# Optimization experiments

Measured on AMD Instinct MI355X. Metric: run time of the kernel, lower is better.

## Reference

```python
import jax, jax.numpy as jnp
import numpy as np

B, S = 8, 128
D_SENS, D_ACT, D_STR, D_ENC, DIM = 512, 32, 128, 128, 128
D_JOINT = D_STR + D_ENC  # 256


def _l2norm(x):
    return x / jnp.clip(jnp.linalg.norm(x, axis=-1, keepdims=True), 1e-12)


def _mlp(x, layers):
    # layers: list of (W, b); ReLU between layers, none on output
    n = len(layers)
    for i, (W, b) in enumerate(layers):
        x = x @ W + b
        if i < n - 1:
            x = jax.nn.relu(x)
    return x


def _meta_mlp(x, p):
    x = jax.nn.relu(x @ p['W1'] + p['b1'])
    x = jax.nn.relu(x @ p['W2'] + p['b2'])
    return x @ p['W3'] + p['b3']


def setup_inputs() -> dict:
    key = jax.random.key(0)
    it = iter(jax.random.split(key, 40))
    w = lambda shape, s=0.02: jax.random.normal(next(it), shape, jnp.float32) * s
    H = D_ACT * 4  # to_transitions hidden dim (default mlp_hidden_dim)
    return dict(
        sensory=jax.random.normal(next(it), (B, S, D_SENS), jnp.float32),
        actions=jax.random.normal(next(it), (B, S, D_ACT), jnp.float32),
        init_hidden=w((1, D_STR), 0.01),
        tW1=w((D_ACT, H)), tb1=w((H,)),
        tW2=w((H, H)), tb2=w((H,)),
        tW3=w((H, D_STR * D_STR)), tb3=w((D_STR * D_STR,)),
        enc_w=w((D_SENS, D_ENC)), enc_b=w((D_ENC,)),
        dec_w=w((D_ENC, D_SENS)), dec_b=w((D_SENS,)),
        q_w=w((D_JOINT, DIM)), k_w=w((D_JOINT, DIM)), v_w=w((D_JOINT, DIM)),
        mW1=w((DIM, 2 * DIM)), mb1=w((2 * DIM,)),
        mW2=w((2 * DIM, 2 * DIM)), mb2=w((2 * DIM,)),
        mW3=w((2 * DIM, DIM)), mb3=w((DIM,)),
        oW1=w((DIM, 2 * DIM)), ob1=w((2 * DIM,)),
        oW2=w((2 * DIM, 2 * DIM)), ob2=w((2 * DIM,)),
        oW3=w((2 * DIM, D_JOINT)), ob3=w((D_JOINT,)),
        sW1=w((2 * D_STR + 1, 2 * D_STR)), sb1=w((2 * D_STR,)),
        sW2=w((2 * D_STR, 2 * D_STR)), sb2=w((2 * D_STR,)),
        sW3=w((2 * D_STR, D_STR)), sb3=w((D_STR,)),
        integration_ratio=jnp.asarray(0.1, jnp.float32),
    )


def reference(sensory, actions, init_hidden, tW1, tb1, tW2, tb2, tW3, tb3,
              enc_w, enc_b, dec_w, dec_b, q_w, k_w, v_w,
              mW1, mb1, mW2, mb2, mW3, mb3,
              oW1, ob1, oW2, ob2, oW3, ob3,
              sW1, sb1, sW2, sb2, sW3, sb3, integration_ratio):
    mse = lambda a, b: jnp.mean((a - b) ** 2)

    # --- PathIntegration: actions -> transitions -> scripted RNN scan ---
    trans = _mlp(actions, [(tW1, tb1), (tW2, tb2), (tW3, tb3)])  # (B,S,ds*ds)
    trans = trans.reshape(B, S, D_STR, D_STR)
    h0 = jnp.broadcast_to(_l2norm(init_hidden), (B, D_STR))

    def step(h, T):  # h (B,ds), T (B,ds,ds)
        h = _l2norm(jax.nn.relu(jnp.einsum('bi,bij->bj', h, T)))
        return h, h

    _, hs = jax.lax.scan(step, h0, jnp.swapaxes(trans, 0, 1))
    structural = jnp.swapaxes(hs, 0, 1)  # (B,S,ds)

    # --- sensory encoder (Linear) ---
    encoded = sensory @ enc_w + enc_b  # (B,S,D_ENC)

    meta_params = {'W1': mW1, 'b1': mb1, 'W2': mW2, 'b2': mb2, 'W3': mW3, 'b3': mb3}

    def retrieve(s, e):
        joint = jnp.concatenate((s, e), axis=-1)
        q = joint @ q_w
        r = _meta_mlp(q, meta_params)
        out = _mlp(r, [(oW1, ob1), (oW2, ob2), (oW3, ob3)])
        return out[..., :D_STR], out[..., D_STR:]

    # generative branch
    dec_gen_s, dec_enc = retrieve(structural, jnp.zeros_like(encoded))
    generative_pred_loss = mse(sensory, dec_enc @ dec_w + dec_b)

    # relational branch (source calls retrieve(zeros, encoded) twice)
    dec_s1, _ = retrieve(jnp.zeros_like(structural), encoded)
    dec_s2, _ = retrieve(jnp.zeros_like(structural), encoded)
    relational_loss = mse(dec_s1, structural) + mse(dec_s2, structural)

    # consistency / inference correction
    corr_s, corr_e = retrieve(dec_gen_s, encoded)
    sse = jnp.sum((corr_e - encoded) ** 2, axis=-1, keepdims=True)  # (B,S,1)
    pred_var = _mlp(jnp.concatenate((corr_s, dec_gen_s, sse), axis=-1),
                    [(sW1, sb1), (sW2, sb2), (sW3, sb3)])
    inf_s = dec_gen_s + (corr_s - dec_gen_s) * integration_ratio * pred_var
    consistency_loss = mse(dec_gen_s, inf_s)

    final_s, inf_e = retrieve(inf_s, jnp.zeros_like(encoded))
    inference_pred_loss = mse(sensory, inf_e @ dec_w + dec_b)

    # per-sample fast-weight memory gradients (nested vmap(grad))
    store = jnp.concatenate((final_s, encoded), axis=-1)
    keys = store @ k_w
    values = store @ v_w

    def meta_loss(p, k, v):
        return jnp.mean((_meta_mlp(k, p) - v) ** 2)

    per_grad = jax.vmap(jax.vmap(jax.grad(meta_loss), in_axes=(None, 0, 0)),
                        in_axes=(None, 0, 0))
    g = per_grad(meta_params, keys, values)  # each leaf (B,S,*param_shape)

    total = (generative_pred_loss + relational_loss
             + consistency_loss + inference_pred_loss)  # all loss weights 1.0
    return (total, g['W1'], g['b1'], g['W2'], g['b2'], g['W3'], g['b3'])
```

## Files before the change

### kernel.cpp

```cpp
#include <hip/hip_runtime.h>
#include <hip/hip_bf16.h>

constexpr size_t OFF_W1 = 1;
constexpr size_t OFF_B1 = OFF_W1 + (size_t)1024*32768;
constexpr size_t OFF_W2 = OFF_B1 + (size_t)1024*256;
constexpr size_t OFF_B2 = OFF_W2 + (size_t)1024*65536;
constexpr size_t OFF_W3 = OFF_B2 + (size_t)1024*256;
constexpr size_t OFF_B3 = OFF_W3 + (size_t)1024*32768;

__device__ __forceinline__ void layer_n256_r8(
    const float* __restrict__ W, const float* __restrict__ bias, int K,
    const float* __restrict__ x, int xs, float* __restrict__ y, int relu, int t)
{
    const int c4 = (t & 63) * 4;
    const int r0 = (t >> 6) * 2;
    float4 a0 = bias ? *(const float4*)&bias[c4] : make_float4(0.f,0.f,0.f,0.f);
    float4 a1 = a0;
    const float* x0 = x + r0 * xs;
    const float* x1 = x0 + xs;
    for (int k = 0; k < K; ++k) {
        float4 w = *(const float4*)&W[(size_t)k*256 + c4];
        float xa = x0[k], xb = x1[k];
        a0.x = fmaf(w.x, xa, a0.x); a0.y = fmaf(w.y, xa, a0.y);
        a0.z = fmaf(w.z, xa, a0.z); a0.w = fmaf(w.w, xa, a0.w);
        a1.x = fmaf(w.x, xb, a1.x); a1.y = fmaf(w.y, xb, a1.y);
        a1.z = fmaf(w.z, xb, a1.z); a1.w = fmaf(w.w, xb, a1.w);
    }
    if (relu) {
        a0.x=fmaxf(a0.x,0.f); a0.y=fmaxf(a0.y,0.f); a0.z=fmaxf(a0.z,0.f); a0.w=fmaxf(a0.w,0.f);
        a1.x=fmaxf(a1.x,0.f); a1.y=fmaxf(a1.y,0.f); a1.z=fmaxf(a1.z,0.f); a1.w=fmaxf(a1.w,0.f);
    }
    *(float4*)&y[r0*256 + c4] = a0;
    *(float4*)&y[(r0+1)*256 + c4] = a1;
}

__device__ __forceinline__ void layer_n256_r4(
    const float* __restrict__ W, const float* __restrict__ bias, int K,
    const float* __restrict__ x, int xs, float* __restrict__ y, int relu,
    const float* __restrict__ mask, int t)
{
    const int c4 = (t & 63) * 4;
    const int r = t >> 6;
    float4 a = bias ? *(const float4*)&bias[c4] : make_float4(0.f,0.f,0.f,0.f);
    const float* xr = x + r * xs;
    for (int k = 0; k < K; ++k) {
        float4 w = *(const float4*)&W[(size_t)k*256 + c4];
        float xa = xr[k];
        a.x = fmaf(w.x, xa, a.x); a.y = fmaf(w.y, xa, a.y);
        a.z = fmaf(w.z, xa, a.z); a.w = fmaf(w.w, xa, a.w);
    }
    if (relu) {
        a.x=fmaxf(a.x,0.f); a.y=fmaxf(a.y,0.f); a.z=fmaxf(a.z,0.f); a.w=fmaxf(a.w,0.f);
    }
    if (mask) {
        float4 m = *(const float4*)&mask[r*256 + c4];
        a.x = (m.x > 0.f) ? a.x : 0.f; a.y = (m.y > 0.f) ? a.y : 0.f;
        a.z = (m.z > 0.f) ? a.z : 0.f; a.w = (m.w > 0.f) ? a.w : 0.f;
    }
    *(float4*)&y[r*256 + c4] = a;
}

__device__ __forceinline__ void layer_n128(
    const float* __restrict__ W, const float* __restrict__ bias, int K,
    const float* __restrict__ x, int xs, float* __restrict__ y, int ys, int relu,
    int rows, int t)
{
    const int c4 = (t & 31) * 4;
    int r = t >> 5; if (rows == 4) r &= 3;
    float4 a = bias ? *(const float4*)&bias[c4] : make_float4(0.f,0.f,0.f,0.f);
    const float* xr = x + r * xs;
    for (int k = 0; k < K; ++k) {
        float4 w = *(const float4*)&W[(size_t)k*128 + c4];
        float xa = xr[k];
        a.x = fmaf(w.x, xa, a.x); a.y = fmaf(w.y, xa, a.y);
        a.z = fmaf(w.z, xa, a.z); a.w = fmaf(w.w, xa, a.w);
    }
    if (relu) {
        a.x=fmaxf(a.x,0.f); a.y=fmaxf(a.y,0.f); a.z=fmaxf(a.z,0.f); a.w=fmaxf(a.w,0.f);
    }
    *(float4*)&y[r*ys + c4] = a;
}

__device__ __forceinline__ void layer_n128_dual(
    const float* __restrict__ W,
    const float* __restrict__ xA, const float* __restrict__ xB,
    float* __restrict__ y, int rows, int t)
{
    const int c4 = (t & 31) * 4;
    int r = t >> 5; if (rows == 4) r &= 3;
    float4 a = make_float4(0.f,0.f,0.f,0.f);
    const float* xa_ = xA + r * 128;
    const float* xb_ = xB + r * 128;
    for (int k = 0; k < 128; ++k) {
        float4 w = *(const float4*)&W[(size_t)k*128 + c4];
        float v = xa_[k];
        a.x = fmaf(w.x, v, a.x); a.y = fmaf(w.y, v, a.y);
        a.z = fmaf(w.z, v, a.z); a.w = fmaf(w.w, v, a.w);
    }
    for (int k = 0; k < 128; ++k) {
        float4 w = *(const float4*)&W[(size_t)(128+k)*128 + c4];
        float v = xb_[k];
        a.x = fmaf(w.x, v, a.x); a.y = fmaf(w.y, v, a.y);
        a.z = fmaf(w.z, v, a.z); a.w = fmaf(w.w, v, a.w);
    }
    *(float4*)&y[r*128 + c4] = a;
}

__device__ __forceinline__ void block_mse_commit(float s, float scale,
                                                 float* __restrict__ accum,
                                                 float* __restrict__ red, int t)
{
    #pragma unroll
    for (int off = 32; off > 0; off >>= 1) s += __shfl_down(s, off, 64);
    if ((t & 63) == 0) red[t >> 6] = s;
    __syncthreads();
    if (t == 0) atomicAdd(accum, (red[0]+red[1]+red[2]+red[3]) * scale);
}

__device__ __forceinline__ void dec_mse(
    const float* __restrict__ ret,
    const float* __restrict__ sensory, int row0,
    const float* __restrict__ dec_w, const float* __restrict__ dec_b,
    float* __restrict__ accum, float* __restrict__ red, int t)
{
    const int c4 = (t & 127) * 4;
    const int rb = (t >> 7) * 2;
    float4 a0 = *(const float4*)&dec_b[c4];
    float4 a1 = a0;
    const float* x0 = ret + rb*256 + 128;
    const float* x1 = x0 + 256;
    for (int k = 0; k < 128; ++k) {
        float4 w = *(const float4*)&dec_w[(size_t)k*512 + c4];
        float xa = x0[k], xb = x1[k];
        a0.x = fmaf(w.x, xa, a0.x); a0.y = fmaf(w.y, xa, a0.y);
        a0.z = fmaf(w.z, xa, a0.z); a0.w = fmaf(w.w, xa, a0.w);
        a1.x = fmaf(w.x, xb, a1.x); a1.y = fmaf(w.y, xb, a1.y);
        a1.z = fmaf(w.z, xb, a1.z); a1.w = fmaf(w.w, xb, a1.w);
    }
    float4 s0 = *(const float4*)&sensory[(size_t)(row0+rb)*512 + c4];
    float4 s1 = *(const float4*)&sensory[(size_t)(row0+rb+1)*512 + c4];
    float dx0 = a0.x-s0.x, dy0 = a0.y-s0.y, dz0 = a0.z-s0.z, dw0 = a0.w-s0.w;
    float dx1 = a1.x-s1.x, dy1 = a1.y-s1.y, dz1 = a1.z-s1.z, dw1 = a1.w-s1.w;
    float s = dx0*dx0 + dy0*dy0 + dz0*dz0 + dw0*dw0
            + dx1*dx1 + dy1*dy1 + dz1*dz1 + dw1*dw1;
    block_mse_commit(s, 1.f/524288.f, accum, red, t);
}

__global__ __launch_bounds__(256) void prep_kernel(
    const float* __restrict__ tW3,
    const float* __restrict__ mW2, const float* __restrict__ mW3,
    const float* __restrict__ actions,
    const float* __restrict__ tW1, const float* __restrict__ tb1,
    const float* __restrict__ tW2, const float* __restrict__ tb2,
    const float* __restrict__ sensory,
    const float* __restrict__ enc_w, const float* __restrict__ enc_b,
    float* __restrict__ tW3T, float* __restrict__ T2, float* __restrict__ T3,
    float* __restrict__ acc, float* __restrict__ a2, float* __restrict__ encoded)
{
    __shared__ float smem[64*129];
    const int t = threadIdx.x;
    const int bid = blockIdx.x;
    if (bid < 256) {
        const int k = bid >> 1, i0 = (bid & 1) * 64;
        const size_t base = (size_t)k << 14;
        for (int l = t; l < 8192; l += 256) {
            int ii = l >> 7, jj = l & 127;
            smem[ii*129 + jj] = tW3[base + (size_t)(i0+ii)*128 + jj];
        }
        __syncthreads();
        for (int l = t; l < 8192; l += 256) {
            int jj = l >> 6, ii = l & 63;
            tW3T[base + (size_t)jj*128 + i0 + ii] = smem[ii*129 + jj];
        }
    } else if (bid < 512) {
        const int c = bid - 256;
        T2[(size_t)c*256 + t] = mW2[(size_t)t*256 + c];
    } else if (bid < 640) {
        const int c = bid - 512;
        T3[(size_t)c*256 + t] = mW3[(size_t)t*128 + c];
    } else if (bid == 640) {
        if (t < 16) acc[t] = 0.f;
    } else if (bid < 769) {
        float* bufAct = smem;
        float* ping   = smem + 256;
        float* pong   = smem + 1280;
        const int row0 = (bid - 641) * 8;
        if (t < 64) {
            int r = t >> 3, c4 = (t & 7) * 4;
            *(float4*)&bufAct[r*32 + c4] =
                *(const float4*)&actions[(size_t)(row0 + r)*32 + c4];
        }
        __syncthreads();
        layer_n128(tW1, tb1, 32, bufAct, 32, ping, 128, 1, 8, t);
        __syncthreads();
        layer_n128(tW2, tb2, 128, ping, 128, pong, 128, 1, 8, t);
        __syncthreads();
        {
            int r = t >> 5, c4 = (t & 31) * 4;
            *(float4*)&a2[(size_t)(row0 + r)*128 + c4] = *(const float4*)&pong[r*128 + c4];
        }
    } else {
        const int q = bid - 769;
        const int m0 = (q & 15) * 64, n0 = (q >> 4) * 64;
        float (*As)[65] = (float(*)[65])smem;
        float (*Ws)[65] = (float(*)[65])(smem + 16*65);
        const int tx = t & 15, ty = t >> 4;
        float a4[4][4] = {};
        for (int k0 = 0; k0 < 512; k0 += 16) {
            for (int l = t; l < 1024; l += 256) {
                int mm = l >> 4, kk = l & 15;
                As[kk][mm] = sensory[(size_t)(m0+mm)*512 + k0 + kk];
            }
            for (int l = t; l < 1024; l += 256) {
                int kk = l >> 6, nn = l & 63;
                Ws[kk][nn] = enc_w[(size_t)(k0+kk)*128 + n0 + nn];
            }
            __syncthreads();
            #pragma unroll
            for (int kk = 0; kk < 16; ++kk) {
                float a[4], b[4];
                #pragma unroll
                for (int i=0;i<4;i++) a[i] = As[kk][ty*4+i];
                #pragma unroll
                for (int j=0;j<4;j++) b[j] = Ws[kk][tx*4+j];
                #pragma unroll
                for (int i=0;i<4;i++)
                    #pragma unroll
                    for (int j=0;j<4;j++)
// ... 60 lines not shown
}

__global__ __launch_bounds__(512) void scanrel_kernel(
    const float* __restrict__ transT,
    const float* __restrict__ init_hidden,
    float* __restrict__ structural,
    const float* __restrict__ encoded,
    const float* __restrict__ qw,
    const float* __restrict__ mW1, const float* __restrict__ mb1,
    const float* __restrict__ mW2, const float* __restrict__ mb2,
    const float* __restrict__ mW3, const float* __restrict__ mb3,
    const float* __restrict__ oW1, const float* __restrict__ ob1,
    const float* __restrict__ oW2, const float* __restrict__ ob2,
    const float* __restrict__ oW3, const float* __restrict__ ob3,
    float* __restrict__ out2)
{
    __shared__ float smem[5120];
    const int tid = threadIdx.x;
    if (blockIdx.x < 8) {
        float* h  = smem;
        float* ws = smem + 128;
        const int b = blockIdx.x;
        const int j = tid >> 2, p = tid & 3;
        const int i0 = p * 32;

        if (tid < 32) {
            float4 v = *(const float4*)&init_hidden[tid*4];
            float ss = v.x*v.x + v.y*v.y + v.z*v.z + v.w*v.w;
            ss += __shfl_xor(ss, 16); ss += __shfl_xor(ss, 8); ss += __shfl_xor(ss, 4);
            ss += __shfl_xor(ss, 2);  ss += __shfl_xor(ss, 1);
            float inv = 1.f / fmaxf(sqrtf(ss), 1e-12f);
            v.x *= inv; v.y *= inv; v.z *= inv; v.w *= inv;
            *(float4*)&h[tid*4] = v;
        }
        __syncthreads();

        const size_t bbase = ((size_t)b) << 21;
        const int lane_off = j*128 + i0;
        float4 cur[8], nxt[8];
        {
            const float* T0 = transT + bbase + lane_off;
            #pragma unroll
            for (int r = 0; r < 8; ++r) cur[r] = *(const float4*)&T0[r*4];
        }
        for (int t = 0; t < 128; ++t) {
            const int tn = (t < 127) ? t + 1 : 127;
            const float* Tn = transT + bbase + ((size_t)tn << 14) + lane_off;
            #pragma unroll
            for (int r = 0; r < 8; ++r) nxt[r] = *(const float4*)&Tn[r*4];

            float4 a = make_float4(0.f, 0.f, 0.f, 0.f);
            #pragma unroll
            for (int r = 0; r < 8; ++r) {
                float4 hv = *(const float4*)&h[i0 + r*4];
                a.x = fmaf(hv.x, cur[r].x, a.x);
                a.y = fmaf(hv.y, cur[r].y, a.y);
                a.z = fmaf(hv.z, cur[r].z, a.z);
                a.w = fmaf(hv.w, cur[r].w, a.w);
            }
            float s = (a.x + a.y) + (a.z + a.w);
            s += __shfl_xor(s, 1);
            s += __shfl_xor(s, 2);
            float v = fmaxf(s, 0.f);
            float q = v * v;
            q += __shfl_xor(q, 4);  q += __shfl_xor(q, 8);
            q += __shfl_xor(q, 16); q += __shfl_xor(q, 32);
            if ((tid & 63) == 0) ws[tid >> 6] = q;
            __syncthreads();
            float ss = ((ws[0]+ws[1]) + (ws[2]+ws[3])) + ((ws[4]+ws[5]) + (ws[6]+ws[7]));
            float inv = 1.f / fmaxf(sqrtf(ss), 1e-12f);
            float hv = v * inv;
            __syncthreads();
            if (p == 0) h[j] = hv;
            else if (p == 1) structural[(((size_t)(b*128 + t)) << 7) + j] = hv;
            __syncthreads();
            #pragma unroll
            for (int r = 0; r < 8; ++r) cur[r] = nxt[r];
        }
    } else {
        float* bufB = smem;
        float* ping = smem + 1024;
        float* pong = smem + 3072;
        const int row0 = (blockIdx.x - 8) * 8;
        const bool act = (tid < 256);
        const int t = tid;
        if (act) {
            int r = t >> 5, k4 = (t & 31) * 4;
            *(float4*)&bufB[r*128 + k4] =
                *(const float4*)&encoded[(size_t)(row0 + r)*128 + k4];
        }
        __syncthreads();
        if (act) layer_n128(qw + (size_t)128*128, nullptr, 128, bufB, 128, ping, 128, 0, 8, t);
        __syncthreads();
        if (act) layer_n256_r8(mW1, mb1, 128, ping, 128, pong, 1, t);
        __syncthreads();
        if (act) layer_n256_r8(mW2, mb2, 256, pong, 256, ping, 1, t);
        __syncthreads();
        if (act) layer_n128(mW3, mb3, 256, ping, 256, pong, 128, 0, 8, t);
        __syncthreads();
        if (act) layer_n256_r8(oW1, ob1, 128, pong, 128, ping, 1, t);
        __syncthreads();
        if (act) layer_n256_r8(oW2, ob2, 256, ping, 256, pong, 1, t);
        __syncthreads();
        if (act) layer_n256_r8(oW3, ob3, 256, pong, 256, ping, 0, t);
        __syncthreads();
        if (act) {
            for (int e = t; e < 512; e += 256) {
                int r = e >> 6, c = (e & 63) * 4;
                *(float4*)&out2[(size_t)(row0+r)*256 + c] = *(const float4*)&ping[r*256 + c];
            }
        }
    }
}

__global__ __launch_bounds__(256) void mega_kernel(
    const float* __restrict__ structural, const float* __restrict__ encoded,
    const float* __restrict__ out2, const float* __restrict__ sensory,
    const float* __restrict__ ratio_p,
    const float* __restrict__ qw,
    const float* __restrict__ mW1, const float* __restrict__ mb1,
    const float* __restrict__ mW2, const float* __restrict__ mb2,
    const float* __restrict__ mW3, const float* __restrict__ mb3,
    const float* __restrict__ oW1, const float* __restrict__ ob1,
    const float* __restrict__ oW2, const float* __restrict__ ob2,
    const float* __restrict__ oW3, const float* __restrict__ ob3,
    const float* __restrict__ sW1, const float* __restrict__ sb1,
    const float* __restrict__ sW2, const float* __restrict__ sb2,
    const float* __restrict__ sW3, const float* __restrict__ sb3,
    const float* __restrict__ k_w, const float* __restrict__ v_w,
    const float* __restrict__ T2, const float* __restrict__ T3,
    const float* __restrict__ dec_w, const float* __restrict__ dec_b,
    float* __restrict__ acc, float* __restrict__ out)
{
    __shared__ float smem[9736];
    float* enc_s    = smem;
    float* struct_s = smem + 512;
    float* ping     = smem + 1024;
    float* pong     = smem + 2048;
    float* ret1     = smem + 3072;
    float* xa128    = smem + 4096;
    float* out3_s   = smem + 4608;
    float* pvar_s   = smem + 5632;
    float* infs_s   = smem + 6144;
    float* ks       = smem + 6656;
    float* vs       = smem + 7168;
    float* h1       = smem + 7680;
    float* h2       = smem + 8704;
    float* sse      = smem + 9728;
    float* red      = smem + 9732;
    const int t = threadIdx.x;
    const int row0 = blockIdx.x * 4;

    {
        int r = (t >> 5) & 3, k4 = (t & 31) * 4;
        *(float4*)&struct_s[r*128 + k4] = *(const float4*)&structural[(size_t)(row0+r)*128 + k4];
        *(float4*)&enc_s[r*128 + k4]    = *(const float4*)&encoded[(size_t)(row0+r)*128 + k4];
    }
    __syncthreads();
    layer_n128(qw, nullptr, 128, struct_s, 128, ping, 128, 0, 4, t); __syncthreads();
    layer_n256_r4(mW1, mb1, 128, ping, 128, pong, 1, nullptr, t); __syncthreads();
    layer_n256_r4(mW2, mb2, 256, pong, 256, ping, 1, nullptr, t); __syncthreads();
    layer_n128(mW3, mb3, 256, ping, 256, pong, 128, 0, 4, t); __syncthreads();
    layer_n256_r4(oW1, ob1, 128, pong, 128, ping, 1, nullptr, t); __syncthreads();
    layer_n256_r4(oW2, ob2, 256, ping, 256, pong, 1, nullptr, t); __syncthreads();
    layer_n256_r4(oW3, ob3, 256, pong, 256, ret1, 0, nullptr, t); __syncthreads();
    {
        float relsum = 0.f;
        for (int e = t; e < 512; e += 256) {
            int r = e >> 7, c = e & 127;
            xa128[e] = ret1[r*256 + c];
            float d = out2[(size_t)(row0+r)*256 + c] - struct_s[r*128 + c];
            relsum = fmaf(d, d, relsum);
        }
        block_mse_commit(relsum, 2.f/131072.f, acc + 1, red, t);
    }
    __syncthreads();
    dec_mse(ret1, sensory, row0, dec_w, dec_b, acc + 0, red, t);
    __syncthreads();
    layer_n128_dual(qw, xa128, enc_s, ping, 4, t); __syncthreads();
    layer_n256_r4(mW1, mb1, 128, ping, 128, pong, 1, nullptr, t); __syncthreads();
    layer_n256_r4(mW2, mb2, 256, pong, 256, ping, 1, nullptr, t); __syncthreads();
    layer_n128(mW3, mb3, 256, ping, 256, pong, 128, 0, 4, t); __syncthreads();
    layer_n256_r4(oW1, ob1, 128, pong, 128, ping, 1, nullptr, t); __syncthreads();
    layer_n256_r4(oW2, ob2, 256, ping, 256, pong, 1, nullptr, t); __syncthreads();
    layer_n256_r4(oW3, ob3, 256, pong, 256, out3_s, 0, nullptr, t); __syncthreads();
    {
        int r = (t >> 5) & 3, k4 = (t & 31) * 4;
        float4 ce = *(const float4*)&out3_s[r*256 + 128 + k4];
        float4 en = *(const float4*)&enc_s[r*128 + k4];
        float dx = ce.x-en.x, dy = ce.y-en.y, dz = ce.z-en.z, dw = ce.w-en.w;
        float ss = dx*dx + dy*dy + dz*dz + dw*dw;
        ss += __shfl_xor(ss, 16); ss += __shfl_xor(ss, 8); ss += __shfl_xor(ss, 4);
        ss += __shfl_xor(ss, 2);  ss += __shfl_xor(ss, 1);
        if ((t & 31) == 0) sse[r] = ss;
    }
    __syncthreads();
    {
        const int c4 = (t & 63) * 4;
        const int r = t >> 6;
        float4 a = *(const float4*)&sb1[c4];
        for (int k = 0; k < 128; ++k) {
            float4 w = *(const float4*)&sW1[(size_t)k*256 + c4];
            float xa = out3_s[r*256 + k];
            a.x=fmaf(w.x,xa,a.x); a.y=fmaf(w.y,xa,a.y); a.z=fmaf(w.z,xa,a.z); a.w=fmaf(w.w,xa,a.w);
        }
        for (int k = 0; k < 128; ++k) {
            float4 w = *(const float4*)&sW1[(size_t)(128+k)*256 + c4];
            float xa = xa128[r*128 + k];
            a.x=fmaf(w.x,xa,a.x); a.y=fmaf(w.y,xa,a.y); a.z=fmaf(w.z,xa,a.z); a.w=fmaf(w.w,xa,a.w);
        }
        {
            float4 w = *(const float4*)&sW1[(size_t)256*256 + c4];
            float xa = sse[r];
            a.x=fmaf(w.x,xa,a.x); a.y=fmaf(w.y,xa,a.y); a.z=fmaf(w.z,xa,a.z); a.w=fmaf(w.w,xa,a.w);
        }
        a.x=fmaxf(a.x,0.f); a.y=fmaxf(a.y,0.f); a.z=fmaxf(a.z,0.f); a.w=fmaxf(a.w,0.f);
        *(float4*)&ping[r*256 + c4] = a;
    }
    __syncthreads();
    layer_n256_r4(sW2, sb2, 256, ping, 256, pong, 1, nullptr, t); __syncthreads();
    layer_n128(sW3, sb3, 256, pong, 256, pvar_s, 128, 0, 4, t); __syncthreads();
    {
        float ratio = ratio_p[0];
        float ssum = 0.f;
        for (int e = t; e < 512; e += 256) {
            int r = e >> 7, j = e & 127;
            float dgs = xa128[r*128 + j];
            float cs  = out3_s[r*256 + j];
            float pv  = pvar_s[r*128 + j];
            float delta = (cs - dgs) * ratio * pv;
            infs_s[r*128 + j] = dgs + delta;
            ssum = fmaf(delta, delta, ssum);
        }
        block_mse_commit(ssum, 1.f/131072.f, acc + 2, red, t);
    }
    __syncthreads();
    layer_n128(qw, nullptr, 128, infs_s, 128, ping, 128, 0, 4, t); __syncthreads();
    layer_n256_r4(mW1, mb1, 128, ping, 128, pong, 1, nullptr, t); __syncthreads();
    layer_n256_r4(mW2, mb2, 256, pong, 256, ping, 1, nullptr, t); __syncthreads();
    layer_n128(mW3, mb3, 256, ping, 256, pong, 128, 0, 4, t); __syncthreads();
    layer_n256_r4(oW1, ob1, 128, pong, 128, ping, 1, nullptr, t); __syncthreads();
    layer_n256_r4(oW2, ob2, 256, ping, 256, pong, 1, nullptr, t); __syncthreads();
    layer_n256_r4(oW3, ob3, 256, pong, 256, ret1, 0, nullptr, t); __syncthreads();
    dec_mse(ret1, sensory, row0, dec_w, dec_b, acc + 3, red, t);
    __syncthreads();
    for (int e = t; e < 512; e += 256) {
        int r = e >> 7, c = e & 127;
        xa128[e] = ret1[r*256 + c];
    }
    __syncthreads();
    float* dob = pvar_s;
    float* dh2 = out3_s;
    float* dh1 = ping;
    layer_n128_dual(k_w, xa128, enc_s, ks, 4, t);
    layer_n128_dual(v_w, xa128, enc_s, vs, 4, t);
    __syncthreads();
    layer_n256_r4(mW1, mb1, 128, ks, 128, h1, 1, nullptr, t);
    __syncthreads();
    layer_n256_r4(mW2, mb2, 256, h1, 256, h2, 1, nullptr, t);
    __syncthreads();
    layer_n128(mW3, mb3, 256, h2, 256, dob, 128, 0, 4, t);
    __syncthreads();
    for (int e = t; e < 512; e += 256)
        dob[e] = (dob[e] - vs[e]) * 0.015625f;
    __syncthreads();
    layer_n256_r4(T3, nullptr, 128, dob, 128, dh2, 0, h2, t);
    __syncthreads();
    layer_n256_r4(T2, nullptr, 256, dh2, 256, dh1, 0, h1, t);
    __syncthreads();
    #pragma unroll
    for (int r = 0; r < 4; ++r) {
        const size_t row = row0 + r;
        {
            const int c4 = (t & 63) * 4;
            const int i0 = (t >> 6) * 32;
            const float4 dv = *(const float4*)&dh1[r*256 + c4];
            float* p = out + OFF_W1 + row*32768;
            for (int i = i0; i < i0 + 32; ++i) {
                float kv = ks[r*128 + i];
                float4 o; o.x = kv*dv.x; o.y = kv*dv.y; o.z = kv*dv.z; o.w = kv*dv.w;
                *(float4*)&p[(size_t)i*256 + c4] = o;
            }
            out[OFF_B1 + row*256 + t] = dh1[r*256 + t];
        }
        {
            const int c4 = (t & 63) * 4;
            const int i0 = (t >> 6) * 64;
            const float4 dv = *(const float4*)&dh2[r*256 + c4];
            float* p = out + OFF_W2 + row*65536;
            for (int i = i0; i < i0 + 64; ++i) {
                float hv = h1[r*256 + i];
                float4 o; o.x = hv*dv.x; o.y = hv*dv.y; o.z = hv*dv.z; o.w = hv*dv.w;
                *(float4*)&p[(size_t)i*256 + c4] = o;
            }
            out[OFF_B2 + row*256 + t] = dh2[r*256 + t];
        }
        {
            const int c4 = (t & 31) * 4;
            const int i0 = (t >> 5) * 32;
            const float4 dv = *(const float4*)&dob[r*128 + c4];
            float* p = out + OFF_W3 + row*32768;
            for (int i = i0; i < i0 + 32; ++i) {
                float hv = h2[r*256 + i];
                float4 o; o.x = hv*dv.x; o.y = hv*dv.y; o.z = hv*dv.z; o.w = hv*dv.w;
                *(float4*)&p[(size_t)i*128 + c4] = o;
            }
            if (t < 128) out[OFF_B3 + row*128 + t] = dob[r*128 + t];
        }
    }
}

__global__ void total_kernel(const float* acc, float* out) {
    if (threadIdx.x == 0)
        out[0] = acc[0] + acc[1] + acc[2] + acc[3];
}

extern "C" void kernel_launch(void* const* d_in, const int* in_sizes, int n_in,
                              void* d_out, int out_size, void* d_ws, size_t ws_size,
                              hipStream_t stream)
{
    const float* sensory     = (const float*)d_in[0];
    const float* actions     = (const float*)d_in[1];
    const float* init_hidden = (const float*)d_in[2];
    const float* tW1 = (const float*)d_in[3];  const float* tb1 = (const float*)d_in[4];
    const float* tW2 = (const float*)d_in[5];  const float* tb2 = (const float*)d_in[6];
    const float* tW3 = (const float*)d_in[7];  const float* tb3 = (const float*)d_in[8];
    const float* enc_w = (const float*)d_in[9];  const float* enc_b = (const float*)d_in[10];
    const float* dec_w = (const float*)d_in[11]; const float* dec_b = (const float*)d_in[12];
    const float* q_w = (const float*)d_in[13];
    const float* k_w = (const float*)d_in[14];
    const float* v_w = (const float*)d_in[15];
    const float* mW1 = (const float*)d_in[16]; const float* mb1 = (const float*)d_in[17];
    const float* mW2 = (const float*)d_in[18]; const float* mb2 = (const float*)d_in[19];
    const float* mW3 = (const float*)d_in[20]; const float* mb3 = (const float*)d_in[21];
    const float* oW1 = (const float*)d_in[22]; const float* ob1 = (const float*)d_in[23];
    const float* oW2 = (const float*)d_in[24]; const float* ob2 = (const float*)d_in[25];
    const float* oW3 = (const float*)d_in[26]; const float* ob3 = (const float*)d_in[27];
    const float* sW1 = (const float*)d_in[28]; const float* sb1 = (const float*)d_in[29];
    const float* sW2 = (const float*)d_in[30]; const float* sb2 = (const float*)d_in[31];
    const float* sW3 = (const float*)d_in[32]; const float* sb3 = (const float*)d_in[33];
    const float* ratio = (const float*)d_in[34];
    float* out = (float*)d_out;

    float* Wsp = (float*)d_ws;
    float* acc   = Wsp;
    float* ALIAS = Wsp + 16;
    float* structural = ALIAS + 131072;
    float* out2 = ALIAS + 524288;
    float* tW3T = ALIAS;
    size_t off = 16 + 2097152;
    float* a2      = Wsp + off; off += 131072;
    float* encoded = Wsp + off; off += 131072;
    float* transT  = Wsp + off; off += 16777216;
    float* T2      = Wsp + off; off += 65536;
    float* T3      = Wsp + off; off += 32768;

    prep_kernel<<<801, 256, 0, stream>>>(tW3, mW2, mW3, actions, tW1, tb1, tW2, tb2,
                                         sensory, enc_w, enc_b, tW3T, T2, T3,
                                         acc, a2, encoded);

    gemm_k128_kernel<<<dim3(32, 64), 256, 0, stream>>>(a2, 128, tW3T, tb3, transT, 16384);

    scanrel_kernel<<<136, 512, 0, stream>>>(transT, init_hidden, structural, encoded,
        q_w, mW1, mb1, mW2, mb2, mW3, mb3, oW1, ob1, oW2, ob2, oW3, ob3, out2);

    mega_kernel<<<256, 256, 0, stream>>>(structural, encoded, out2, sensory, ratio,
        q_w, mW1, mb1, mW2, mb2, mW3, mb3, oW1, ob1, oW2, ob2, oW3, ob3,
        sW1, sb1, sW2, sb2, sW3, sb3, k_w, v_w, T2, T3, dec_w, dec_b, acc, out);

    total_kernel<<<1, 64, 0, stream>>>(acc, out);
}
```

Measured before the change: 1.321 ms.

## Double mega_kernel threads with split-K layers and widen scanrel MLP to 512 threads

Launches mega_kernel with 512 threads per block and splits each small MLP layer's K dimension across 2 or 4 thread groups, reducing partial sums through shared memory. In scanrel, the 8-row MLP layers now use all 512 threads, one row per thread, instead of 256 threads handling two rows each. The decoder MSE and the gradient outer-product writes are spread over the wider block. The aim is more latency hiding and parallelism on a grid of only 256 blocks, at the cost of extra shared memory, extra barriers and reduction work per layer.

```diff
diff --git a/kernel.cpp b/kernel.cpp
--- a/kernel.cpp
+++ b/kernel.cpp
@@ -8,36 +8,30 @@
 constexpr size_t OFF_W3 = OFF_B2 + (size_t)1024*256;
 constexpr size_t OFF_B3 = OFF_W3 + (size_t)1024*32768;
 
-__device__ __forceinline__ void layer_n256_r8(
+__device__ __forceinline__ void layer_n128(
+    const float* __restrict__ W, const float* __restrict__ bias, int K,
+    const float* __restrict__ x, int xs, float* __restrict__ y, int ys, int relu,
+    int rows, int t)
+{
+    const int c4 = (t & 31) * 4;
+    int r = t >> 5; if (rows == 4) r &= 3;
+    float4 a = bias ? *(const float4*)&bias[c4] : make_float4(0.f,0.f,0.f,0.f);
+    const float* xr = x + r * xs;
+    for (int k = 0; k < K; ++k) {
+        float4 w = *(const float4*)&W[(size_t)k*128 + c4];
+        float xa = xr[k];
+        a.x = fmaf(w.x, xa, a.x); a.y = fmaf(w.y, xa, a.y);
+        a.z = fmaf(w.z, xa, a.z); a.w = fmaf(w.w, xa, a.w);
+    }
+    if (relu) {
+        a.x=fmaxf(a.x,0.f); a.y=fmaxf(a.y,0.f); a.z=fmaxf(a.z,0.f); a.w=fmaxf(a.w,0.f);
+    }
+    *(float4*)&y[r*ys + c4] = a;
+}
+
+__device__ __forceinline__ void layer_n256_512(
     const float* __restrict__ W, const float* __restrict__ bias, int K,
     const float* __restrict__ x, int xs, float* __restrict__ y, int relu, int t)
-{
-    const int c4 = (t & 63) * 4;
-    const int r0 = (t >> 6) * 2;
-    float4 a0 = bias ? *(const float4*)&bias[c4] : make_float4(0.f,0.f,0.f,0.f);
-    float4 a1 = a0;
-    const float* x0 = x + r0 * xs;
-    const float* x1 = x0 + xs;
-    for (int k = 0; k < K; ++k) {
-        float4 w = *(const float4*)&W[(size_t)k*256 + c4];
-        float xa = x0[k], xb = x1[k];
-        a0.x = fmaf(w.x, xa, a0.x); a0.y = fmaf(w.y, xa, a0.y);
-        a0.z = fmaf(w.z, xa, a0.z); a0.w = fmaf(w.w, xa, a0.w);
-        a1.x = fmaf(w.x, xb, a1.x); a1.y = fmaf(w.y, xb, a1.y);
-        a1.z = fmaf(w.z, xb, a1.z); a1.w = fmaf(w.w, xb, a1.w);
-    }
-    if (relu) {
-        a0.x=fmaxf(a0.x,0.f); a0.y=fmaxf(a0.y,0.f); a0.z=fmaxf(a0.z,0.f); a0.w=fmaxf(a0.w,0.f);
-        a1.x=fmaxf(a1.x,0.f); a1.y=fmaxf(a1.y,0.f); a1.z=fmaxf(a1.z,0.f); a1.w=fmaxf(a1.w,0.f);
-    }
-    *(float4*)&y[r0*256 + c4] = a0;
-    *(float4*)&y[(r0+1)*256 + c4] = a1;
-}
-
-__device__ __forceinline__ void layer_n256_r4(
-    const float* __restrict__ W, const float* __restrict__ bias, int K,
-    const float* __restrict__ x, int xs, float* __restrict__ y, int relu,
-    const float* __restrict__ mask, int t)
 {
     const int c4 = (t & 63) * 4;
     const int r = t >> 6;
@@ -52,98 +46,159 @@
     if (relu) {
         a.x=fmaxf(a.x,0.f); a.y=fmaxf(a.y,0.f); a.z=fmaxf(a.z,0.f); a.w=fmaxf(a.w,0.f);
     }
-    if (mask) {
-        float4 m = *(const float4*)&mask[r*256 + c4];
-        a.x = (m.x > 0.f) ? a.x : 0.f; a.y = (m.y > 0.f) ? a.y : 0.f;
-        a.z = (m.z > 0.f) ? a.z : 0.f; a.w = (m.w > 0.f) ? a.w : 0.f;
-    }
     *(float4*)&y[r*256 + c4] = a;
 }
 
-__device__ __forceinline__ void layer_n128(
+__device__ __forceinline__ void layer_ks2_n256(
+    const float* __restrict__ W, const float* __restrict__ bias, int K,
+    const float* __restrict__ x, int xs, float* __restrict__ y, int relu,
+    const float* __restrict__ mask, float* __restrict__ part, int t)
+{
+    const int g = t >> 8;
+    const int tt = t & 255;
+    const int r = tt >> 6, c4 = (tt & 63) * 4;
+    const int kh = K >> 1;
+    const int kb = g * kh;
+    float4 a = make_float4(0.f,0.f,0.f,0.f);
+    const float* xr = x + r * xs;
+    for (int k = kb; k < kb + kh; ++k) {
+        float4 w = *(const float4*)&W[(size_t)k*256 + c4];
+        float xa = xr[k];
+        a.x = fmaf(w.x, xa, a.x); a.y = fmaf(w.y, xa, a.y);
+        a.z = fmaf(w.z, xa, a.z); a.w = fmaf(w.w, xa, a.w);
+    }
+    *(float4*)&part[g*1024 + tt*4] = a;
+    __syncthreads();
+    if (g == 0) {
+        float4 p0 = *(const float4*)&part[tt*4];
+        float4 p1 = *(const float4*)&part[1024 + tt*4];
+        float4 o;
+        o.x = p0.x + p1.x; o.y = p0.y + p1.y; o.z = p0.z + p1.z; o.w = p0.w + p1.w;
+        if (bias) {
+            float4 b = *(const float4*)&bias[c4];
+            o.x += b.x; o.y += b.y; o.z += b.z; o.w += b.w;
+        }
+        if (relu) {
+            o.x=fmaxf(o.x,0.f); o.y=fmaxf(o.y,0.f); o.z=fmaxf(o.z,0.f); o.w=fmaxf(o.w,0.f);
+        }
+        if (mask) {
+            float4 m = *(const float4*)&mask[r*256 + c4];
+            o.x = (m.x > 0.f) ? o.x : 0.f; o.y = (m.y > 0.f) ? o.y : 0.f;
+            o.z = (m.z > 0.f) ? o.z : 0.f; o.w = (m.w > 0.f) ? o.w : 0.f;
+        }
+        *(float4*)&y[r*256 + c4] = o;
+    }
+    __syncthreads();
+}
+
+__device__ __forceinline__ void layer_ks4_n128(
     const float* __restrict__ W, const float* __restrict__ bias, int K,
     const float* __restrict__ x, int xs, float* __restrict__ y, int ys, int relu,
-    int rows, int t)
-{
-    const int c4 = (t & 31) * 4;
-    int r = t >> 5; if (rows == 4) r &= 3;
-    float4 a = bias ? *(const float4*)&bias[c4] : make_float4(0.f,0.f,0.f,0.f);
+    float* __restrict__ part, int t)
+{
+    const int g = t >> 7;
+    const int tt = t & 127;
+    const int r = tt >> 5, c4 = (tt & 31) * 4;
+    const int kq = K >> 2;
+    const int kb = g * kq;
+    float4 a = make_float4(0.f,0.f,0.f,0.f);
     const float* xr = x + r * xs;
-    for (int k = 0; k < K; ++k) {
+    for (int k = kb; k < kb + kq; ++k) {
         float4 w = *(const float4*)&W[(size_t)k*128 + c4];
         float xa = xr[k];
         a.x = fmaf(w.x, xa, a.x); a.y = fmaf(w.y, xa, a.y);
         a.z = fmaf(w.z, xa, a.z); a.w = fmaf(w.w, xa, a.w);
     }
-    if (relu) {
-        a.x=fmaxf(a.x,0.f); a.y=fmaxf(a.y,0.f); a.z=fmaxf(a.z,0.f); a.w=fmaxf(a.w,0.f);
-    }
-    *(float4*)&y[r*ys + c4] = a;
-}
-
-__device__ __forceinline__ void layer_n128_dual(
+    *(float4*)&part[g*512 + tt*4] = a;
+    __syncthreads();
+    if (g == 0) {
+        float4 p0 = *(const float4*)&part[tt*4];
+        float4 p1 = *(const float4*)&part[512 + tt*4];
+        float4 p2 = *(const float4*)&part[1024 + tt*4];
+        float4 p3 = *(const float4*)&part[1536 + tt*4];
+        float4 o;
+        o.x = (p0.x+p1.x) + (p2.x+p3.x); o.y = (p0.y+p1.y) + (p2.y+p3.y);
+        o.z = (p0.z+p1.z) + (p2.z+p3.z); o.w = (p0.w+p1.w) + (p2.w+p3.w);
+        if (bias) {
+            float4 b = *(const float4*)&bias[c4];
+            o.x += b.x; o.y += b.y; o.z += b.z; o.w += b.w;
+        }
+        if (relu) {
+            o.x=fmaxf(o.x,0.f); o.y=fmaxf(o.y,0.f); o.z=fmaxf(o.z,0.f); o.w=fmaxf(o.w,0.f);
+        }
+        *(float4*)&y[r*ys + c4] = o;
+    }
+    __syncthreads();
+}
+
+__device__ __forceinline__ void layer_ks4_n128_dual(
     const float* __restrict__ W,
     const float* __restrict__ xA, const float* __restrict__ xB,
-    float* __restrict__ y, int rows, int t)
-{
-    const int c4 = (t & 31) * 4;
-    int r = t >> 5; if (rows == 4) r &= 3;
+    float* __restrict__ y, float* __restrict__ part, int t)
+{
+    const int g = t >> 7;
+    const int tt = t & 127;
+    const int r = tt >> 5, c4 = (tt & 31) * 4;
+    const float* src = (g < 2) ? xA : xB;
+    const int kb = (g & 1) * 64;
+    const int wb = g * 64;
     float4 a = make_float4(0.f,0.f,0.f,0.f);
-    const float* xa_ = xA + r * 128;
-    const float* xb_ = xB + r * 128;
-    for (int k = 0; k < 128; ++k) {
-        float4 w = *(const float4*)&W[(size_t)k*128 + c4];
-        float v = xa_[k];
-        a.x = fmaf(w.x, v, a.x); a.y = fmaf(w.y, v, a.y);
-        a.z = fmaf(w.z, v, a.z); a.w = fmaf(w.w, v, a.w);
-    }
-    for (int k = 0; k < 128; ++k) {
-        float4 w = *(const float4*)&W[(size_t)(128+k)*128 + c4];
-        float v = xb_[k];
-        a.x = fmaf(w.x, v, a.x); a.y = fmaf(w.y, v, a.y);
-        a.z = fmaf(w.z, v, a.z); a.w = fmaf(w.w, v, a.w);
-    }
-    *(float4*)&y[r*128 + c4] = a;
-}
-
-__device__ __forceinline__ void block_mse_commit(float s, float scale,
-                                                 float* __restrict__ accum,
-                                                 float* __restrict__ red, int t)
+    const float* xr = src + r * 128;
+    for (int k = 0; k < 64; ++k) {
+        float4 w = *(const float4*)&W[(size_t)(wb + k)*128 + c4];
+        float xa = xr[kb + k];
+        a.x = fmaf(w.x, xa, a.x); a.y = fmaf(w.y, xa, a.y);
+        a.z = fmaf(w.z, xa, a.z); a.w = fmaf(w.w, xa, a.w);
+    }
+    *(float4*)&part[g*512 + tt*4] = a;
+    __syncthreads();
+    if (g == 0) {
+        float4 p0 = *(const float4*)&part[tt*4];
+        float4 p1 = *(const float4*)&part[512 + tt*4];
+        float4 p2 = *(const float4*)&part[1024 + tt*4];
+        float4 p3 = *(const float4*)&part[1536 + tt*4];
+        float4 o;
+        o.x = (p0.x+p1.x) + (p2.x+p3.x); o.y = (p0.y+p1.y) + (p2.y+p3.y);
+        o.z = (p0.z+p1.z) + (p2.z+p3.z); o.w = (p0.w+p1.w) + (p2.w+p3.w);
+        *(float4*)&y[r*128 + c4] = o;
+    }
+    __syncthreads();
+}
+
+__device__ __forceinline__ void block_mse_commit512(float s, float scale,
+                                                    float* __restrict__ accum,
+                                                    float* __restrict__ red, int t)
 {
     #pragma unroll
     for (int off = 32; off > 0; off >>= 1) s += __shfl_down(s, off, 64);
     if ((t & 63) == 0) red[t >> 6] = s;
     __syncthreads();
-    if (t == 0) atomicAdd(accum, (red[0]+red[1]+red[2]+red[3]) * scale);
-}
-
-__device__ __forceinline__ void dec_mse(
+    if (t == 0) {
+        float tot = ((red[0]+red[1]) + (red[2]+red[3])) + ((red[4]+red[5]) + (red[6]+red[7]));
+        atomicAdd(accum, tot * scale);
+    }
+}
+
+__device__ __forceinline__ void dec_mse512(
     const float* __restrict__ ret,
     const float* __restrict__ sensory, int row0,
     const float* __restrict__ dec_w, const float* __restrict__ dec_b,
     float* __restrict__ accum, float* __restrict__ red, int t)
 {
     const int c4 = (t & 127) * 4;
-    const int rb = (t >> 7) * 2;
-    float4 a0 = *(const float4*)&dec_b[c4];
-    float4 a1 = a0;
+    const int rb = t >> 7;
+    float4 a = *(const float4*)&dec_b[c4];
     const float* x0 = ret + rb*256 + 128;
-    const float* x1 = x0 + 256;
     for (int k = 0; k < 128; ++k) {
         float4 w = *(const float4*)&dec_w[(size_t)k*512 + c4];
-        float xa = x0[k], xb = x1[k];
-        a0.x = fmaf(w.x, xa, a0.x); a0.y = fmaf(w.y, xa, a0.y);
-        a0.z = fmaf(w.z, xa, a0.z); a0.w = fmaf(w.w, xa, a0.w);
-        a1.x = fmaf(w.x, xb, a1.x); a1.y = fmaf(w.y, xb, a1.y);
-        a1.z = fmaf(w.z, xb, a1.z); a1.w = fmaf(w.w, xb, a1.w);
+        float xa = x0[k];
+        a.x = fmaf(w.x, xa, a.x); a.y = fmaf(w.y, xa, a.y);
+        a.z = fmaf(w.z, xa, a.z); a.w = fmaf(w.w, xa, a.w);
     }
     float4 s0 = *(const float4*)&sensory[(size_t)(row0+rb)*512 + c4];
-    float4 s1 = *(const float4*)&sensory[(size_t)(row0+rb+1)*512 + c4];
-    float dx0 = a0.x-s0.x, dy0 = a0.y-s0.y, dz0 = a0.z-s0.z, dw0 = a0.w-s0.w;
-    float dx1 = a1.x-s1.x, dy1 = a1.y-s1.y, dz1 = a1.z-s1.z, dw1 = a1.w-s1.w;
-    float s = dx0*dx0 + dy0*dy0 + dz0*dz0 + dw0*dw0
-            + dx1*dx1 + dy1*dy1 + dz1*dz1 + dw1*dw1;
-    block_mse_commit(s, 1.f/524288.f, accum, red, t);
+    float dx = a.x-s0.x, dy = a.y-s0.y, dz = a.z-s0.z, dw = a.w-s0.w;
+    float s = dx*dx + dy*dy + dz*dz + dw*dw;
+    block_mse_commit512(s, 1.f/524288.f, accum, red, t);
 }
 
 __global__ __launch_bounds__(256) void prep_kernel(
@@ -370,38 +425,35 @@
         float* ping = smem + 1024;
         float* pong = smem + 3072;
         const int row0 = (blockIdx.x - 8) * 8;
-        const bool act = (tid < 256);
         const int t = tid;
-        if (act) {
+        if (t < 256) {
             int r = t >> 5, k4 = (t & 31) * 4;
             *(float4*)&bufB[r*128 + k4] =
                 *(const float4*)&encoded[(size_t)(row0 + r)*128 + k4];
         }
         __syncthreads();
-        if (act) layer_n128(qw + (size_t)128*128, nullptr, 128, bufB, 128, ping, 128, 0, 8, t);
-        __syncthreads();
-        if (act) layer_n256_r8(mW1, mb1, 128, ping, 128, pong, 1, t);
-        __syncthreads();
-        if (act) layer_n256_r8(mW2, mb2, 256, pong, 256, ping, 1, t);
-        __syncthreads();
-        if (act) layer_n128(mW3, mb3, 256, ping, 256, pong, 128, 0, 8, t);
-        __syncthreads();
-        if (act) layer_n256_r8(oW1, ob1, 128, pong, 128, ping, 1, t);
-        __syncthreads();
-        if (act) layer_n256_r8(oW2, ob2, 256, ping, 256, pong, 1, t);
-        __syncthreads();
-        if (act) layer_n256_r8(oW3, ob3, 256, pong, 256, ping, 0, t);
-        __syncthreads();
-        if (act) {
-            for (int e = t; e < 512; e += 256) {
-                int r = e >> 6, c = (e & 63) * 4;
-                *(float4*)&out2[(size_t)(row0+r)*256 + c] = *(const float4*)&ping[r*256 + c];
-            }
-        }
-    }
-}
-
-__global__ __launch_bounds__(256) void mega_kernel(
+        if (t < 256) layer_n128(qw + (size_t)128*128, nullptr, 128, bufB, 128, ping, 128, 0, 8, t);
+        __syncthreads();
+        layer_n256_512(mW1, mb1, 128, ping, 128, pong, 1, t);
+        __syncthreads();
+        layer_n256_512(mW2, mb2, 256, pong, 256, ping, 1, t);
+        __syncthreads();
+        if (t < 256) layer_n128(mW3, mb3, 256, ping, 256, pong, 128, 0, 8, t);
+        __syncthreads();
+        layer_n256_512(oW1, ob1, 128, pong, 128, ping, 1, t);
+        __syncthreads();
+        layer_n256_512(oW2, ob2, 256, ping, 256, pong, 1, t);
+        __syncthreads();
+        layer_n256_512(oW3, ob3, 256, pong, 256, ping, 0, t);
+        __syncthreads();
+        {
+            int r = t >> 6, c = (t & 63) * 4;
+            *(float4*)&out2[(size_t)(row0+r)*256 + c] = *(const float4*)&ping[r*256 + c];
+        }
+    }
+}
+
+__global__ __launch_bounds__(512) void mega_kernel(
     const float* __restrict__ structural, const float* __restrict__ encoded,
     const float* __restrict__ out2, const float* __restrict__ sensory,
     const float* __restrict__ ratio_p,
@@ -420,7 +472,7 @@
     const float* __restrict__ dec_w, const float* __restrict__ dec_b,
     float* __restrict__ acc, float* __restrict__ out)
 {
-    __shared__ float smem[9736];
+    __shared__ float smem[11788];
     float* enc_s    = smem;
     float* struct_s = smem + 512;
     float* ping     = smem + 1024;
@@ -434,45 +486,43 @@
     float* vs       = smem + 7168;
     float* h1       = smem + 7680;
     float* h2       = smem + 8704;
-    float* sse      = smem + 9728;
-    float* red      = smem + 9732;
+    float* part     = smem + 9728;
+    float* sse      = smem + 11776;
+    float* red      = smem + 11780;
     const int t = threadIdx.x;
     const int row0 = blockIdx.x * 4;
 
-    {
+    if (t < 256) {
         int r = (t >> 5) & 3, k4 = (t & 31) * 4;
         *(float4*)&struct_s[r*128 + k4] = *(const float4*)&structural[(size_t)(row0+r)*128 + k4];
         *(float4*)&enc_s[r*128 + k4]    = *(const float4*)&encoded[(size_t)(row0+r)*128 + k4];
     }
     __syncthreads();
-    layer_n128(qw, nullptr, 128, struct_s, 128, ping, 128, 0, 4, t); __syncthreads();
-    layer_n256_r4(mW1, mb1, 128, ping, 128, pong, 1, nullptr, t); __syncthreads();
-    layer_n256_r4(mW2, mb2, 256, pong, 256, ping, 1, nullptr, t); __syncthreads();
-    layer_n128(mW3, mb3, 256, ping, 256, pong, 128, 0, 4, t); __syncthreads();
-    layer_n256_r4(oW1, ob1, 128, pong, 128, ping, 1, nullptr, t); __syncthreads();
-    layer_n256_r4(oW2, ob2, 256, ping, 256, pong, 1, nullptr, t); __syncthreads();
-    layer_n256_r4(oW3, ob3, 256, pong, 256, ret1, 0, nullptr, t); __syncthreads();
+    layer_ks4_n128(qw, nullptr, 128, struct_s, 128, ping, 128, 0, part, t);
+    layer_ks2_n256(mW1, mb1, 128, ping, 128, pong, 1, nullptr, part, t);
+    layer_ks2_n256(mW2, mb2, 256, pong, 256, ping, 1, nullptr, part, t);
+    layer_ks4_n128(mW3, mb3, 256, ping, 256, pong, 128, 0, part, t);
+    layer_ks2_n256(oW1, ob1, 128, pong, 128, ping, 1, nullptr, part, t);
+    layer_ks2_n256(oW2, ob2, 256, ping, 256, pong, 1, nullptr, part, t);
+    layer_ks2_n256(oW3, ob3, 256, pong, 256, ret1, 0, nullptr, part, t);
     {
-        float relsum = 0.f;
-        for (int e = t; e < 512; e += 256) {
-            int r = e >> 7, c = e & 127;
-            xa128[e] = ret1[r*256 + c];
-            float d = out2[(size_t)(row0+r)*256 + c] - struct_s[r*128 + c];
-            relsum = fmaf(d, d, relsum);
-        }
-        block_mse_commit(relsum, 2.f/131072.f, acc + 1, red, t);
-    }
-    __syncthreads();
-    dec_mse(ret1, sensory, row0, dec_w, dec_b, acc + 0, red, t);
-    __syncthreads();
-    layer_n128_dual(qw, xa128, enc_s, ping, 4, t); __syncthreads();
-    layer_n256_r4(mW1, mb1, 128, ping, 128, pong, 1, nullptr, t); __syncthreads();
-    layer_n256_r4(mW2, mb2, 256, pong, 256, ping, 1, nullptr, t); __syncthreads();
-    layer_n128(mW3, mb3, 256, ping, 256, pong, 128, 0, 4, t); __syncthreads();
-    layer_n256_r4(oW1, ob1, 128, pong, 128, ping, 1, nullptr, t); __syncthreads();
-    layer_n256_r4(oW2, ob2, 256, ping, 256, pong, 1, nullptr, t); __syncthreads();
-    layer_n256_r4(oW3, ob3, 256, pong, 256, out3_s, 0, nullptr, t); __syncthreads();
-    {
+        const int r = t >> 7, c = t & 127;
+        xa128[t] = ret1[r*256 + c];
+        float d = out2[(size_t)(row0+r)*256 + c] - struct_s[r*128 + c];
+        float relsum = d * d;
+        block_mse_commit512(relsum, 2.f/131072.f, acc + 1, red, t);
+    }
+    __syncthreads();
+    dec_mse512(ret1, sensory, row0, dec_w, dec_b, acc + 0, red, t);
+    __syncthreads();
+    layer_ks4_n128_dual(qw, xa128, enc_s, ping, part, t);
+    layer_ks2_n256(mW1, mb1, 128, ping, 128, pong, 1, nullptr, part, t);
+    layer_ks2_n256(mW2, mb2, 256, pong, 256, ping, 1, nullptr, part, t);
+    layer_ks4_n128(mW3, mb3, 256, ping, 256, pong, 128, 0, part, t);
+    layer_ks2_n256(oW1, ob1, 128, pong, 128, ping, 1, nullptr, part, t);
+    layer_ks2_n256(oW2, ob2, 256, ping, 256, pong, 1, nullptr, part, t);
+    layer_ks2_n256(oW3, ob3, 256, pong, 256, out3_s, 0, nullptr, part, t);
+    if (t < 256) {
         int r = (t >> 5) & 3, k4 = (t & 31) * 4;
         float4 ce = *(const float4*)&out3_s[r*256 + 128 + k4];
         float4 en = *(const float4*)&enc_s[r*128 + k4];
@@ -484,111 +534,113 @@
     }
     __syncthreads();
     {
-        const int c4 = (t & 63) * 4;
-        const int r = t >> 6;
-        float4 a = *(const float4*)&sb1[c4];
-        for (int k = 0; k < 128; ++k) {
-            float4 w = *(const float4*)&sW1[(size_t)k*256 + c4];
-            float xa = out3_s[r*256 + k];
-            a.x=fmaf(w.x,xa,a.x); a.y=fmaf(w.y,xa,a.y); a.z=fmaf(w.z,xa,a.z); a.w=fmaf(w.w,xa,a.w);
-        }
-        for (int k = 0; k < 128; ++k) {
-            float4 w = *(const float4*)&sW1[(size_t)(128+k)*256 + c4];
-            float xa = xa128[r*128 + k];
-            a.x=fmaf(w.x,xa,a.x); a.y=fmaf(w.y,xa,a.y); a.z=fmaf(w.z,xa,a.z); a.w=fmaf(w.w,xa,a.w);
-        }
-        {
+        const int g = t >> 8;
+        const int tt = t & 255;
+        const int r = tt >> 6, c4 = (tt & 63) * 4;
+        float4 a = make_float4(0.f,0.f,0.f,0.f);
+        if (g == 0) {
+            for (int k = 0; k < 128; ++k) {
+                float4 w = *(const float4*)&sW1[(size_t)k*256 + c4];
+                float xa = out3_s[r*256 + k];
+                a.x=fmaf(w.x,xa,a.x); a.y=fmaf(w.y,xa,a.y); a.z=fmaf(w.z,xa,a.z); a.w=fmaf(w.w,xa,a.w);
+            }
+        } else {
+            for (int k = 0; k < 128; ++k) {
+                float4 w = *(const float4*)&sW1[(size_t)(128+k)*256 + c4];
+                float xa = xa128[r*128 + k];
+                a.x=fmaf(w.x,xa,a.x); a.y=fmaf(w.y,xa,a.y); a.z=fmaf(w.z,xa,a.z); a.w=fmaf(w.w,xa,a.w);
+            }
             float4 w = *(const float4*)&sW1[(size_t)256*256 + c4];
             float xa = sse[r];
             a.x=fmaf(w.x,xa,a.x); a.y=fmaf(w.y,xa,a.y); a.z=fmaf(w.z,xa,a.z); a.w=fmaf(w.w,xa,a.w);
         }
-        a.x=fmaxf(a.x,0.f); a.y=fmaxf(a.y,0.f); a.z=fmaxf(a.z,0.f); a.w=fmaxf(a.w,0.f);
-        *(float4*)&ping[r*256 + c4] = a;
-    }
-    __syncthreads();
-    layer_n256_r4(sW2, sb2, 256, ping, 256, pong, 1, nullptr, t); __syncthreads();
-    layer_n128(sW3, sb3, 256, pong, 256, pvar_s, 128, 0, 4, t); __syncthreads();
+        *(float4*)&part[g*1024 + tt*4] = a;
+        __syncthreads();
+        if (g == 0) {
+            float4 p0 = *(const float4*)&part[tt*4];
+            float4 p1 = *(const float4*)&part[1024 + tt*4];
+            float4 b  = *(const float4*)&sb1[c4];
+            float4 o;
+            o.x = fmaxf(p0.x + p1.x + b.x, 0.f);
+            o.y = fmaxf(p0.y + p1.y + b.y, 0.f);
+            o.z = fmaxf(p0.z + p1.z + b.z, 0.f);
+            o.w = fmaxf(p0.w + p1.w + b.w, 0.f);
+            *(float4*)&ping[r*256 + c4] = o;
+        }
+        __syncthreads();
+    }
+    layer_ks2_n256(sW2, sb2, 256, ping, 256, pong, 1, nullptr, part, t);
+    layer_ks4_n128(sW3, sb3, 256, pong, 256, pvar_s, 128, 0, part, t);
     {
         float ratio = ratio_p[0];
-        float ssum = 0.f;
-        for (int e = t; e < 512; e += 256) {
-            int r = e >> 7, j = e & 127;
-            float dgs = xa128[r*128 + j];
-            float cs  = out3_s[r*256 + j];
-            float pv  = pvar_s[r*128 + j];
-            float delta = (cs - dgs) * ratio * pv;
-            infs_s[r*128 + j] = dgs + delta;
-            ssum = fmaf(delta, delta, ssum);
-        }
-        block_mse_commit(ssum, 1.f/131072.f, acc + 2, red, t);
-    }
-    __syncthreads();
-    layer_n128(qw, nullptr, 128, infs_s, 128, ping, 128, 0, 4, t); __syncthreads();
-    layer_n256_r4(mW1, mb1, 128, ping, 128, pong, 1, nullptr, t); __syncthreads();
-    layer_n256_r4(mW2, mb2, 256, pong, 256, ping, 1, nullptr, t); __syncthreads();
-    layer_n128(mW3, mb3, 256, ping, 256, pong, 128, 0, 4, t); __syncthreads();
-    layer_n256_r4(oW1, ob1, 128, pong, 128, ping, 1, nullptr, t); __syncthreads();
-    layer_n256_r4(oW2, ob2, 256, ping, 256, pong, 1, nullptr, t); __syncthreads();
-    layer_n256_r4(oW3, ob3, 256, pong, 256, ret1, 0, nullptr, t); __syncthreads();
-    dec_mse(ret1, sensory, row0, dec_w, dec_b, acc + 3, red, t);
-    __syncthreads();
-    for (int e = t; e < 512; e += 256) {
-        int r = e >> 7, c = e & 127;
-        xa128[e] = ret1[r*256 + c];
+        const int r = t >> 7, j = t & 127;
+        float dgs = xa128[t];
+        float cs  = out3_s[r*256 + j];
+        float pv  = pvar_s[t];
+        float delta = (cs - dgs) * ratio * pv;
+        infs_s[t] = dgs + delta;
+        block_mse_commit512(delta * delta, 1.f/131072.f, acc + 2, red, t);
+    }
+    __syncthreads();
+    layer_ks4_n128(qw, nullptr, 128, infs_s, 128, ping, 128, 0, part, t);
+    layer_ks2_n256(mW1, mb1, 128, ping, 128, pong, 1, nullptr, part, t);
+    layer_ks2_n256(mW2, mb2, 256, pong, 256, ping, 1, nullptr, part, t);
+    layer_ks4_n128(mW3, mb3, 256, ping, 256, pong, 128, 0, part, t);
+    layer_ks2_n256(oW1, ob1, 128, pong, 128, ping, 1, nullptr, part, t);
+    layer_ks2_n256(oW2, ob2, 256, ping, 256, pong, 1, nullptr, part, t);
+    layer_ks2_n256(oW3, ob3, 256, pong, 256, ret1, 0, nullptr, part, t);
+    dec_mse512(ret1, sensory, row0, dec_w, dec_b, acc + 3, red, t);
+    __syncthreads();
+    {
+        const int r = t >> 7, c = t & 127;
+        xa128[t] = ret1[r*256 + c];
     }
     __syncthreads();
     float* dob = pvar_s;
     float* dh2 = out3_s;
     float* dh1 = ping;
-    layer_n128_dual(k_w, xa128, enc_s, ks, 4, t);
-    layer_n128_dual(v_w, xa128, enc_s, vs, 4, t);
-    __syncthreads();
-    layer_n256_r4(mW1, mb1, 128, ks, 128, h1, 1, nullptr, t);
-    __syncthreads();
-    layer_n256_r4(mW2, mb2, 256, h1, 256, h2, 1, nullptr, t);
-    __syncthreads();
-    layer_n128(mW3, mb3, 256, h2, 256, dob, 128, 0, 4, t);
-    __syncthreads();
-    for (int e = t; e < 512; e += 256)
-        dob[e] = (dob[e] - vs[e]) * 0.015625f;
-    __syncthreads();
-    layer_n256_r4(T3, nullptr, 128, dob, 128, dh2, 0, h2, t);
-    __syncthreads();
-    layer_n256_r4(T2, nullptr, 256, dh2, 256, dh1, 0, h1, t);
-    __syncthreads();
+    layer_ks4_n128_dual(k_w, xa128, enc_s, ks, part, t);
+    layer_ks4_n128_dual(v_w, xa128, enc_s, vs, part, t);
+    layer_ks2_n256(mW1, mb1, 128, ks, 128, h1, 1, nullptr, part, t);
+    layer_ks2_n256(mW2, mb2, 256, h1, 256, h2, 1, nullptr, part, t);
+    layer_ks4_n128(mW3, mb3, 256, h2, 256, dob, 128, 0, part, t);
+    dob[t] = (dob[t] - vs[t]) * 0.015625f;
+    __syncthreads();
+    layer_ks2_n256(T3, nullptr, 128, dob, 128, dh2, 0, h2, part, t);
+    layer_ks2_n256(T2, nullptr, 256, dh2, 256, dh1, 0, h1, part, t);
     #pragma unroll
     for (int r = 0; r < 4; ++r) {
         const size_t row = row0 + r;
         {
             const int c4 = (t & 63) * 4;
-            const int i0 = (t >> 6) * 32;
+            const int i0 = (t >> 6) * 16;
             const float4 dv = *(const float4*)&dh1[r*256 + c4];
             float* p = out + OFF_W1 + row*32768;
-            for (int i = i0; i < i0 + 32; ++i) {
+            for (int i = i0; i < i0 + 16; ++i) {
                 float kv = ks[r*128 + i];
                 float4 o; o.x = kv*dv.x; o.y = kv*dv.y; o.z = kv*dv.z; o.w = kv*dv.w;
                 *(float4*)&p[(size_t)i*256 + c4] = o;
             }
-            out[OFF_B1 + row*256 + t] = dh1[r*256 + t];
+            if (t < 256) out[OFF_B1 + row*256 + t] = dh1[r*256 + t];
         }
         {
             const int c4 = (t & 63) * 4;
-            const int i0 = (t >> 6) * 64;
+            const int i0 = (t >> 6) * 32;
             const float4 dv = *(const float4*)&dh2[r*256 + c4];
             float* p = out + OFF_W2 + row*65536;
-            for (int i = i0; i < i0 + 64; ++i) {
+            for (int i = i0; i < i0 + 32; ++i) {
                 float hv = h1[r*256 + i];
                 float4 o; o.x = hv*dv.x; o.y = hv*dv.y; o.z = hv*dv.z; o.w = hv*dv.w;
                 *(float4*)&p[(size_t)i*256 + c4] = o;
             }
-            out[OFF_B2 + row*256 + t] = dh2[r*256 + t];
+            if (t < 256) out[OFF_B2 + row*256 + t] = dh2[r*256 + t];
         }
         {
             const int c4 = (t & 31) * 4;
-            const int i0 = (t >> 5) * 32;
+            const int i0 = (t >> 5) * 16;
             const float4 dv = *(const float4*)&dob[r*128 + c4];
             float* p = out + OFF_W3 + row*32768;
-            for (int i = i0; i < i0 + 32; ++i) {
+            for (int i = i0; i < i0 + 16; ++i) {
                 float hv = h2[r*256 + i];
                 float4 o; o.x = hv*dv.x; o.y = hv*dv.y; o.z = hv*dv.z; o.w = hv*dv.w;
                 *(float4*)&p[(size_t)i*128 + c4] = o;
@@ -652,7 +704,7 @@
     scanrel_kernel<<<136, 512, 0, stream>>>(transT, init_hidden, structural, encoded,
         q_w, mW1, mb1, mW2, mb2, mW3, mb3, oW1, ob1, oW2, ob2, oW3, ob3, out2);
 
-    mega_kernel<<<256, 256, 0, stream>>>(structural, encoded, out2, sensory, ratio,
+    mega_kernel<<<256, 512, 0, stream>>>(structural, encoded, out2, sensory, ratio,
         q_w, mW1, mb1, mW2, mb2, mW3, mb3, oW1, ob1, oW2, ob2, oW3, ob3,
         sW1, sb1, sW2, sb2, sW3, sb3, k_w, v_w, T2, T3, dec_w, dec_b, acc, out);
 
```

Result: slower. 1.880 ms (+42.3%).
